# Optimization experiments

Measured on AMD Instinct MI355X. Metric: run time of the kernel, lower is better.

The kernel has to match this reference:

```python
import math
import jax, jax.numpy as jnp
import numpy as np

N, E, D, H, NH, DH, EIN, EOUT, G = 30000, 480000, 128, 128, 4, 32, 16, 16, 64
EPS = 1e-5

def _leaky(x):
    return jax.nn.leaky_relu(x, 0.01)

def _graph_norm(x, batch, w, b, a):
    # torch_geometric GraphNorm: out = w * (x - a*mean) / sqrt(var + eps) + b, stats per graph
    cnt = jnp.maximum(jax.ops.segment_sum(jnp.ones((x.shape[0],), x.dtype), batch, num_segments=G), 1.0)[:, None]
    mean = jax.ops.segment_sum(x, batch, num_segments=G) / cnt
    out = x - a * mean[batch]
    var = jax.ops.segment_sum(out * out, batch, num_segments=G) / cnt
    return w * out / jnp.sqrt(var + EPS)[batch] + b

def setup_inputs() -> dict:
    key = jax.random.key(0)
    ks = jax.random.split(key, 24)
    lin = lambda k, di, do: jax.random.normal(k, (di, do), jnp.float32) * 0.02
    z = lambda d: jnp.zeros((d,), jnp.float32)
    o = lambda d: jnp.ones((d,), jnp.float32)
    return {
        "node": jax.random.normal(ks[0], (N, D), jnp.float32),
        "edge": jax.random.normal(ks[1], (E, EIN), jnp.float32),
        "coords": jax.random.normal(ks[2], (N, 3), jnp.float32),
        "Ws": lin(ks[3], D, H), "bs": z(H),
        "Wd": lin(ks[4], D, H), "bd": z(H),
        "Wv": lin(ks[5], D, H), "bv": z(H),
        "We1": lin(ks[6], EIN + 1, H), "be1": z(H),
        "We2": lin(ks[7], H, H), "be2": z(H),
        "Wun": lin(ks[8], H, H), "bun": z(H),
        "Wue": lin(ks[9], H, EOUT), "bue": z(EOUT),
        "Wg": lin(ks[10], 3 * H, H), "bg": z(H),
        "Wf1": lin(ks[11], H, H), "bf1": z(H),
        "Wf2": lin(ks[12], H, H), "bf2": z(H),
        "gn1_w": o(H), "gn1_b": z(H), "gn1_a": o(H),
        "gn2_w": o(H), "gn2_b": z(H), "gn2_a": o(H),
        "edge_index": jax.random.randint(ks[13], (2, E), 0, N),
        "batch": jnp.sort(jax.random.randint(ks[14], (N,), 0, G)),
    }

def reference(node, edge, coords, Ws, bs, Wd, bd, Wv, bv, We1, be1, We2, be2,
              Wun, bun, Wue, bue, Wg, bg, Wf1, bf1, Wf2, bf2,
              gn1_w, gn1_b, gn1_a, gn2_w, gn2_b, gn2_a, edge_index, batch):
    i, j = edge_index[0], edge_index[1]
    src = node @ Ws + bs              # [N,H]
    dst = node @ Wd + bd
    value = node @ Wv + bv
    d = coords[i] - coords[j]
    dist = jnp.sqrt(jnp.sum(d * d, axis=-1, keepdims=True) + 1e-12) * 0.1
    e = jnp.concatenate([edge, dist], axis=-1)            # [E, EIN+1]
    e = _leaky(e @ We1 + be1) @ We2 + be2                   # edge_layer (dropout=identity in eval)
    edge_key = src[j] * e
    edge_result = (dst[i] * edge_key / math.sqrt(DH)).reshape(E, NH, DH)
    scores = jnp.sum(jnp.abs(edge_result), axis=2)         # L1 norm over dh -> [E,NH]
    smax = jax.ops.segment_max(scores, i, num_segments=N)  # scatter softmax over dst nodes
    ex = jnp.exp(scores - smax[i])
    den = jax.ops.segment_sum(ex, i, num_segments=N)
    ew = (ex / den[i])[..., None]                           # [E,NH,1]
    agg = jax.ops.segment_sum(ew * value[j].reshape(E, NH, DH), i, num_segments=N).reshape(N, H)
    node_new = agg @ Wun + bun
    edge_new = edge_result.reshape(E, H) @ Wue + bue
    g = jax.nn.sigmoid(jnp.concatenate([node_new, node, node_new - node], axis=-1) @ Wg + bg)
    n1 = _graph_norm(g * node_new + node, batch, gn1_w, gn1_b, gn1_a)
    fx = _leaky(n1 @ Wf1 + bf1) @ Wf2 + bf2                 # fix_node
    n2 = _graph_norm(g * fx + n1, batch, gn2_w, gn2_b, gn2_a)
    return (n2, edge_new, coords)
```

## Files before the change

kernel.cpp:

```cpp
#include <hip/hip_runtime.h>
#include <hip/hip_bf16.h>

#define NN_ 30000
#define NE_ 480000
#define DIM 128
#define EINF 16
#define EOUTF 16
#define NG 64
#define RSQRT_DH 0.17677669529663687f

typedef unsigned short u16;
typedef __attribute__((ext_vector_type(8))) short short8;
typedef __attribute__((ext_vector_type(8))) unsigned short ushort8v;
typedef __attribute__((ext_vector_type(4))) float floatx4;

#define W_DEG     0
#define W_CUR     30000
#define W_GSUM1   60000
#define W_GSQ1    68192
#define W_GSUM2   76384
#define W_GSQ2    84576
#define W_ZEND    92768
#define W_OFF     92768
#define W_BSUM    122772
#define W_GSTART  122900
#define W_EID     122968
#define W_JC      602968
#define W_SCORES  1082968
#define W_SRCB    3002968
#define W_DSTB    4922968
#define W_VALB    6842968
#define W_A       8762968
#define W_B       12602968
#define W_C       16442968
#define W_WGC     20282968
#define W_WE2B    20315736

static __device__ __forceinline__ u16 f2bf(float x) {
  __hip_bfloat16 h = __float2bfloat16(x);
  return *reinterpret_cast<u16*>(&h);
}
static __device__ __forceinline__ float bf2f(u16 v) {
  unsigned int b = ((unsigned int)v) << 16;
  return __uint_as_float(b);
}

static __device__ __forceinline__ void stage32(const float* __restrict__ X,
                                               float* xsb, int row0, int tid) {
#pragma unroll
  for (int t = 0; t < 4; ++t) {
    int idx = tid + t * 256;
    int r = idx >> 5, c4 = (idx & 31) * 4;
    int row = row0 + r;
    float4 v; v.x = v.y = v.z = v.w = 0.f;
    if (row < NN_) v = *(const float4*)&X[(size_t)row * DIM + c4];
    *(float4*)&xsb[r * DIM + c4] = v;
  }
}

static __device__ __forceinline__ void mm_k128(const float* xsb, int ld,
                                               const float* __restrict__ W,
                                               float acc[4][4], int tid) {
  int cg = tid & 31, rg = tid >> 5;
  int c0 = cg * 4, r0 = rg * 4;
  for (int k = 0; k < 128; k += 4) {
    float4 w0 = *(const float4*)&W[(size_t)(k + 0) * DIM + c0];
    float4 w1 = *(const float4*)&W[(size_t)(k + 1) * DIM + c0];
    float4 w2 = *(const float4*)&W[(size_t)(k + 2) * DIM + c0];
    float4 w3 = *(const float4*)&W[(size_t)(k + 3) * DIM + c0];
#pragma unroll
    for (int u = 0; u < 4; ++u) {
      float4 xv = *(const float4*)&xsb[(r0 + u) * ld + k];
      acc[u][0] += xv.x * w0.x + xv.y * w1.x + xv.z * w2.x + xv.w * w3.x;
      acc[u][1] += xv.x * w0.y + xv.y * w1.y + xv.z * w2.y + xv.w * w3.y;
      acc[u][2] += xv.x * w0.z + xv.y * w1.z + xv.z * w2.z + xv.w * w3.z;
      acc[u][3] += xv.x * w0.w + xv.y * w1.w + xv.z * w2.w + xv.w * w3.w;
    }
  }
}

static __device__ __forceinline__ void epi_store_bf(float acc[4][4],
    const float* __restrict__ bias, u16* __restrict__ Y,
    int row0, int tid) {
  int cg = tid & 31, rg = tid >> 5;
  int c0 = cg * 4, r0 = rg * 4;
  float4 bv = *(const float4*)&bias[c0];
#pragma unroll
  for (int u = 0; u < 4; ++u) {
    int row = row0 + r0 + u;
    if (row >= NN_) continue;
    ushort4 pk;
    pk.x = f2bf(acc[u][0] + bv.x); pk.y = f2bf(acc[u][1] + bv.y);
    pk.z = f2bf(acc[u][2] + bv.z); pk.w = f2bf(acc[u][3] + bv.w);
    *(ushort4*)&Y[(size_t)row * DIM + c0] = pk;
  }
}

static __device__ __forceinline__ void tile_gn_stats(const float* xsb,
    const int* bg_s, int row0, int tid,
    float* __restrict__ gsum, float* __restrict__ gsq) {
  int c = tid & 127, half = tid >> 7;
  float sm = 0.f, sq = 0.f;
  int gcur = -1;
  for (int r = 0; r < 16; ++r) {
    int rl = half * 16 + r;
    int row = row0 + rl;
    if (row >= NN_) break;
    int g = bg_s[rl];
    float v = xsb[rl * DIM + c];
    if (g != gcur) {
      if (gcur >= 0) {
        atomicAdd(&gsum[gcur * DIM + c], sm);
        atomicAdd(&gsq[gcur * DIM + c], sq);
      }
      gcur = g; sm = 0.f; sq = 0.f;
    }
    sm += v; sq += v * v;
  }
  if (gcur >= 0) {
    atomicAdd(&gsum[gcur * DIM + c], sm);
    atomicAdd(&gsq[gcur * DIM + c], sq);
  }
}

__global__ void setup_kernel(int* __restrict__ wsi, const int* __restrict__ batch,
                             int* __restrict__ gstart,
                             const float* __restrict__ Wg, float* __restrict__ Wgc,
                             const float* __restrict__ We2, u16* __restrict__ we2b) {
  int b = blockIdx.x, tid = threadIdx.x;
  if (b < 363) {
    int i = b * 256 + tid;
    if (i < W_ZEND) wsi[i] = 0;
  } else if (b == 363) {
    int g = tid;
    if (g <= NG) {
      int lo = 0, hi = NN_;
      while (lo < hi) { int mid = (lo + hi) >> 1; if (batch[mid] < g) lo = mid + 1; else hi = mid; }
      gstart[g] = lo;
    }
  } else if (b < 492) {
    int idx = (b - 364) * 256 + tid;
    int k = idx >> 7, c = idx & 127;
    float v;
    if (k < 128) v = Wg[(size_t)k * DIM + c] + Wg[(size_t)(256 + k) * DIM + c];
    else { int kk = k - 128; v = Wg[(size_t)(128 + kk) * DIM + c] - Wg[(size_t)(256 + kk) * DIM + c]; }
    Wgc[idx] = v;
  } else {
    int idx = (b - 492) * 256 + tid;
    if (idx < 16384) {
      int j = idx & 7, lane = (idx >> 3) & 63, s = (idx >> 9) & 3, T = idx >> 11;
      int k = s * 32 + ((lane >> 4) << 3) + j;
      int n = T * 16 + (lane & 15);
      we2b[idx] = f2bf(We2[(size_t)k * DIM + n]);
    }
  }
}

__global__ void deg_kernel(const int* __restrict__ EI, int* __restrict__ deg) {
  int e = blockIdx.x * 256 + threadIdx.x;
  if (e < NE_) atomicAdd(&deg[EI[e]], 1);
}

__global__ void __launch_bounds__(256) proj_kernel(
    const float* __restrict__ node,
    const float* __restrict__ Ws, const float* __restrict__ bs,
    const float* __restrict__ Wd, const float* __restrict__ bd,
    const float* __restrict__ Wv, const float* __restrict__ bv,
    u16* __restrict__ srcb, u16* __restrict__ dstb, u16* __restrict__ valb) {
  __shared__ __align__(16) float xs[32 * DIM];
  int tid = threadIdx.x, row0 = blockIdx.x * 32;
  stage32(node, xs, row0, tid);
  __syncthreads();
  const float* Wt[3] = {Ws, Wd, Wv};
  const float* Bt[3] = {bs, bd, bv};
  u16* Yt[3] = {srcb, dstb, valb};
#pragma unroll
  for (int w3 = 0; w3 < 3; ++w3) {
    float acc[4][4] = {};
    mm_k128(xs, DIM, Wt[w3], acc, tid);
    epi_store_bf(acc, Bt[w3], Yt[w3], row0, tid);
  }
}

__global__ void __launch_bounds__(256) nnew_gate_kernel(
    const float* __restrict__ AGG, const float* __restrict__ NODE,
    const int* __restrict__ batch,
    const float* __restrict__ Wun, const float* __restrict__ bun,
    const float* __restrict__ Wgc, const float* __restrict__ bg,
    float* __restrict__ gsum1, float* __restrict__ gsq1,
    float* __restrict__ G, float* __restrict__ X1) {
  __shared__ __align__(16) float xs0[32 * DIM];
  __shared__ __align__(16) float xs1[32 * DIM];
  __shared__ int bg_s[32];
  int tid = threadIdx.x, row0 = blockIdx.x * 32;
  stage32(AGG, xs0, row0, tid);
  stage32(NODE, xs1, row0, tid);
  if (tid < 32) {
    int row = row0 + tid;
    bg_s[tid] = (row < NN_) ? batch[row] : 0;
  }
  __syncthreads();
  int cg = tid & 31, rg = tid >> 5, c0 = cg * 4, r0 = rg * 4;
  {
    float acc[4][4] = {};
    mm_k128(xs0, DIM, Wun, acc, tid);
    __syncthreads();
    float4 bv = *(const float4*)&bun[c0];
#pragma unroll
    for (int u = 0; u < 4; ++u) {
      float4 ov; ov.x = acc[u][0] + bv.x; ov.y = acc[u][1] + bv.y;
      ov.z = acc[u][2] + bv.z; ov.w = acc[u][3] + bv.w;
      *(float4*)&xs0[(r0 + u) * DIM + c0] = ov;
    }
  }
  __syncthreads();
  float acc[4][4] = {};
  mm_k128(xs0, DIM, Wgc, acc, tid);
  mm_k128(xs1, DIM, Wgc + 128 * DIM, acc, tid);
  float4 bv = *(const float4*)&bg[c0];
  float4 xvv[4];
#pragma unroll
  for (int u = 0; u < 4; ++u) {
    int row = row0 + r0 + u;
    float z0 = acc[u][0] + bv.x, z1 = acc[u][1] + bv.y;
    float z2 = acc[u][2] + bv.z, z3 = acc[u][3] + bv.w;
    float g0 = 1.f / (1.f + __expf(-z0));
    float g1 = 1.f / (1.f + __expf(-z1));
    float g2 = 1.f / (1.f + __expf(-z2));
    float g3 = 1.f / (1.f + __expf(-z3));
    float4 nn4 = *(const float4*)&xs0[(r0 + u) * DIM + c0];
    float4 nd4 = *(const float4*)&xs1[(r0 + u) * DIM + c0];
    float4 gv; gv.x = g0; gv.y = g1; gv.z = g2; gv.w = g3;
    float4 xv; xv.x = g0 * nn4.x + nd4.x; xv.y = g1 * nn4.y + nd4.y;
    xv.z = g2 * nn4.z + nd4.z; xv.w = g3 * nn4.w + nd4.w;
    xvv[u] = xv;
    if (row < NN_) {
      *(float4*)&G[(size_t)row * DIM + c0] = gv;
      *(float4*)&X1[(size_t)row * DIM + c0] = xv;
    }
  }
  __syncthreads();
#pragma unroll
  for (int u = 0; u < 4; ++u)
    *(float4*)&xs1[(r0 + u) * DIM + c0] = xvv[u];
  __syncthreads();
  tile_gn_stats(xs1, bg_s, row0, tid, gsum1, gsq1);
}

__global__ void __launch_bounds__(256) fx_kernel(
    const float* __restrict__ X1, const int* __restrict__ batch,
    const int* __restrict__ gstart,
    const float* __restrict__ gsum1, const float* __restrict__ gsq1,
    const float* __restrict__ g1w, const float* __restrict__ g1b,
    const float* __restrict__ g1a,
    const float* __restrict__ Wf1, const float* __restrict__ bf1,
    const float* __restrict__ Wf2, const float* __restrict__ bf2,
    const float* __restrict__ G,
    float* __restrict__ gsum2, float* __restrict__ gsq2,
    float* __restrict__ X2) {
  __shared__ __align__(16) float xs0[32 * DIM];
  __shared__ __align__(16) float xs1[32 * DIM];
  __shared__ int bg_s[32];
  int tid = threadIdx.x, row0 = blockIdx.x * 32;
  stage32(X1, xs0, row0, tid);
  if (tid < 32) {
    int row = row0 + tid;
    bg_s[tid] = (row < NN_) ? batch[row] : 0;
  }
  __syncthreads();
  int cg = tid & 31, rg = tid >> 5, c0 = cg * 4, r0 = rg * 4;
#pragma unroll
  for (int u = 0; u < 4; ++u) {
    int rl = r0 + u, row = row0 + rl;
    if (row >= NN_) continue;
    int g = bg_s[rl];
    float cnt = fmaxf((float)(gstart[g + 1] - gstart[g]), 1.f);
    float inv = 1.f / cnt;
    float4 xv = *(const float4*)&xs0[rl * DIM + c0];
    float4 sm = *(const float4*)&gsum1[g * DIM + c0];
    float4 sq = *(const float4*)&gsq1[g * DIM + c0];
    float4 av = *(const float4*)&g1a[c0];
    float4 wv = *(const float4*)&g1w[c0];
    float4 bvv = *(const float4*)&g1b[c0];
    float4 ov;
    {
      float mean = sm.x * inv, msq = sq.x * inv, am = av.x * mean;
      float var = msq - 2.f * am * mean + am * am;
      ov.x = wv.x * (xv.x - am) * rsqrtf(var + 1e-5f) + bvv.x;
    }
    {
      float mean = sm.y * inv, msq = sq.y * inv, am = av.y * mean;
      float var = msq - 2.f * am * mean + am * am;
      ov.y = wv.y * (xv.y - am) * rsqrtf(var + 1e-5f) + bvv.y;
    }
    {
      float mean = sm.z * inv, msq = sq.z * inv, am = av.z * mean;
      float var = msq - 2.f * am * mean + am * am;
      ov.z = wv.z * (xv.z - am) * rsqrtf(var + 1e-5f) + bvv.z;
    }
    {
      float mean = sm.w * inv, msq = sq.w * inv, am = av.w * mean;
      float var = msq - 2.f * am * mean + am * am;
      ov.w = wv.w * (xv.w - am) * rsqrtf(var + 1e-5f) + bvv.w;
    }
    *(float4*)&xs0[rl * DIM + c0] = ov;
  }
  __syncthreads();
  {
    float acc[4][4] = {};
    mm_k128(xs0, DIM, Wf1, acc, tid);
    float4 bv = *(const float4*)&bf1[c0];
#pragma unroll
    for (int u = 0; u < 4; ++u) {
      float t0 = acc[u][0] + bv.x, t1 = acc[u][1] + bv.y;
      float t2 = acc[u][2] + bv.z, t3 = acc[u][3] + bv.w;
      t0 = t0 > 0.f ? t0 : 0.01f * t0; t1 = t1 > 0.f ? t1 : 0.01f * t1;
      t2 = t2 > 0.f ? t2 : 0.01f * t2; t3 = t3 > 0.f ? t3 : 0.01f * t3;
      float4 ov; ov.x = t0; ov.y = t1; ov.z = t2; ov.w = t3;
      *(float4*)&xs1[(r0 + u) * DIM + c0] = ov;
    }
  }
  __syncthreads();
  float acc[4][4] = {};
  mm_k128(xs1, DIM, Wf2, acc, tid);
  float4 bv = *(const float4*)&bf2[c0];
  float4 x2v[4];
#pragma unroll
  for (int u = 0; u < 4; ++u) {
    int row = row0 + r0 + u;
    float4 nv = *(const float4*)&xs0[(r0 + u) * DIM + c0];
    float4 gv; gv.x = gv.y = gv.z = gv.w = 0.f;
    if (row < NN_) gv = *(const float4*)&G[(size_t)row * DIM + c0];
    float4 ov;
    ov.x = gv.x * (acc[u][0] + bv.x) + nv.x;
    ov.y = gv.y * (acc[u][1] + bv.y) + nv.y;
    ov.z = gv.z * (acc[u][2] + bv.z) + nv.z;
    ov.w = gv.w * (acc[u][3] + bv.w) + nv.w;
    x2v[u] = ov;
    if (row < NN_) *(float4*)&X2[(size_t)row * DIM + c0] = ov;
  }
  __syncthreads();
#pragma unroll
  for (int u = 0; u < 4; ++u)
    *(float4*)&xs1[(r0 + u) * DIM + c0] = x2v[u];
  __syncthreads();
  tile_gn_stats(xs1, bg_s, row0, tid, gsum2, gsq2);
}

__global__ void scanA_kernel(const int* __restrict__ deg, int* __restrict__ off,
                             int* __restrict__ bsum) {
  __shared__ int buf[256];
  int tid = threadIdx.x;
  int i = blockIdx.x * 256 + tid;
  int v = (i < NN_) ? deg[i] : 0;
  buf[tid] = v;
  __syncthreads();
  for (int s = 1; s < 256; s <<= 1) {
    int t = (tid >= s) ? buf[tid - s] : 0;
    __syncthreads();
    buf[tid] += t;
    __syncthreads();
  }
  if (i < NN_) off[i] = buf[tid] - v;
  if (tid == 255) bsum[blockIdx.x] = buf[255];
}

__global__ void scanB_kernel(int* __restrict__ bsum) {
  const int NBLK = (NN_ + 255) / 256;
  __shared__ int buf[128];
  int tid = threadIdx.x;
  int v = (tid < NBLK) ? bsum[tid] : 0;
  buf[tid] = v;
  __syncthreads();
  for (int s = 1; s < 128; s <<= 1) {
    int t = (tid >= s) ? buf[tid - s] : 0;
    __syncthreads();
    buf[tid] += t;
    __syncthreads();
  }
  if (tid < NBLK) bsum[tid] = buf[tid] - v;
}

__global__ void scanC_kernel(int* __restrict__ off, const int* __restrict__ bsum) {
  int i = blockIdx.x * 256 + threadIdx.x;
  if (i < NN_) off[i] += bsum[i >> 8];
  if (i == 0) off[NN_] = NE_;
}

__global__ void fill_kernel(const int* __restrict__ EI, const int* __restrict__ off,
                            int* __restrict__ cur, int* __restrict__ eidb,
                            int* __restrict__ jcsr) {
  int e = blockIdx.x * 256 + threadIdx.x;
  if (e >= NE_) return;
  int i = EI[e];
  int p = atomicAdd(&cur[i], 1);
  int pos = off[i] + p;
  eidb[pos] = e;
  jcsr[pos] = EI[NE_ + e];
}

__global__ void __launch_bounds__(256, 5) edge_kernel(
    const float* __restrict__ edgef, const float* __restrict__ coords,
    const int* __restrict__ EI, const int* __restrict__ eidb,
    const float* __restrict__ We1, const float* __restrict__ be1,
    const float* __restrict__ be2, const u16* __restrict__ we2b,
    const float* __restrict__ Wue, const float* __restrict__ bue,
    const u16* __restrict__ srcb, const u16* __restrict__ dstb,
    float* __restrict__ scores, float* __restrict__ outE) {
  __shared__ __align__(16) float regA[2816];
  __shared__ __align__(16) float ers[32 * 132];
  __shared__ float bue_s[EOUTF];
  __shared__ int ii[32], jj[32], ee[32];

  float* xs   = regA;
  u16*   hbf  = (u16*)(regA + 640);
  float* wue_s= regA;

  int tid = threadIdx.x;
  int bid = blockIdx.x;
  int bswz = (bid & 7) * (NE_ / 32 / 8) + (bid >> 3);
  int p0 = bswz * 32;

  if (tid < 32) {
    int p = p0 + tid;
    int e = eidb[p];
    ee[tid] = e;
    int i = EI[e], j = EI[NE_ + e];
    ii[tid] = i; jj[tid] = j;
    float dx = coords[i * 3 + 0] - coords[j * 3 + 0];
    float dy = coords[i * 3 + 1] - coords[j * 3 + 1];
    float dz = coords[i * 3 + 2] - coords[j * 3 + 2];
    float dist = sqrtf(dx * dx + dy * dy + dz * dz + 1e-12f) * 0.1f;
    xs[tid * 20 + 16] = dist;
  }
  if (tid < EOUTF) bue_s[tid] = bue[tid];
  __syncthreads();

  if (tid < 128) {
    int r = tid >> 2, c4 = (tid & 3) * 4;
    *(float4*)&xs[r * 20 + c4] = *(const float4*)&edgef[(size_t)ee[r] * EINF + c4];
  }
  __syncthreads();

  int cg = tid & 31, rg = tid >> 5, c0 = cg * 4, r0 = rg * 4;

  {
    float acc[4][4] = {};
    for (int k = 0; k < 16; k += 4) {
      float4 w0 = *(const float4*)&We1[(size_t)(k + 0) * DIM + c0];
      float4 w1 = *(const float4*)&We1[(size_t)(k + 1) * DIM + c0];
      float4 w2 = *(const float4*)&We1[(size_t)(k + 2) * DIM + c0];
      float4 w3 = *(const float4*)&We1[(size_t)(k + 3) * DIM + c0];
#pragma unroll
      for (int u = 0; u < 4; ++u) {
        float4 xv = *(const float4*)&xs[(r0 + u) * 20 + k];
        acc[u][0] += xv.x * w0.x + xv.y * w1.x + xv.z * w2.x + xv.w * w3.x;
        acc[u][1] += xv.x * w0.y + xv.y * w1.y + xv.z * w2.y + xv.w * w3.y;
        acc[u][2] += xv.x * w0.z + xv.y * w1.z + xv.z * w2.z + xv.w * w3.z;
        acc[u][3] += xv.x * w0.w + xv.y * w1.w + xv.z * w2.w + xv.w * w3.w;
      }
    }
    {
      float4 w4 = *(const float4*)&We1[(size_t)16 * DIM + c0];
#pragma unroll
      for (int u = 0; u < 4; ++u) {
        float xd = xs[(r0 + u) * 20 + 16];
        acc[u][0] += xd * w4.x; acc[u][1] += xd * w4.y;
        acc[u][2] += xd * w4.z; acc[u][3] += xd * w4.w;
      }
    }
    float4 b1 = *(const float4*)&be1[c0];
#pragma unroll
    for (int u = 0; u < 4; ++u) {
      float h0 = acc[u][0] + b1.x, h1 = acc[u][1] + b1.y;
      float h2 = acc[u][2] + b1.z, h3 = acc[u][3] + b1.w;
      h0 = h0 > 0.f ? h0 : 0.01f * h0; h1 = h1 > 0.f ? h1 : 0.01f * h1;
      h2 = h2 > 0.f ? h2 : 0.01f * h2; h3 = h3 > 0.f ? h3 : 0.01f * h3;
      ushort4 pk; pk.x = f2bf(h0); pk.y = f2bf(h1); pk.z = f2bf(h2); pk.w = f2bf(h3);
      *(ushort4*)&hbf[(r0 + u) * 136 + c0] = pk;
    }
  }
  __syncthreads();

  int wv = tid >> 6, lane = tid & 63;
  int mtile = wv & 1, nhalf = wv >> 1;
  int quad = lane >> 4, lrow = lane & 15;
  int m0 = mtile * 16;

  short8 afrag[4];
#pragma unroll
  for (int s = 0; s < 4; ++s)
    afrag[s] = *(const short8*)&hbf[(m0 + lrow) * 136 + s * 32 + quad * 8];
  __syncthreads();

  for (int idx = tid; idx < 16 * DIM; idx += 256) {
    int oc = idx >> 7, k = idx & 127;
    wue_s[oc * 132 + k] = Wue[(size_t)k * EOUTF + oc];
  }

  floatx4 dacc[4];
#pragma unroll
  for (int t = 0; t < 4; ++t) dacc[t] = (floatx4){0.f, 0.f, 0.f, 0.f};
#pragma unroll
  for (int s = 0; s < 4; ++s) {
#pragma unroll
    for (int t = 0; t < 4; ++t) {
      int T = nhalf * 4 + t;
      short8 bfrg = *(const short8*)&we2b[(size_t)((T * 4 + s) * 64 + lane) * 8];
      dacc[t] = __builtin_amdgcn_mfma_f32_16x16x32_bf16(afrag[s], bfrg, dacc[t], 0, 0, 0);
    }
  }

#pragma unroll
  for (int t = 0; t < 4; ++t) {
    int col = nhalf * 64 + t * 16 + lrow;
    float b2v = be2[col];
#pragma unroll
    for (int r = 0; r < 4; ++r) {
      int erow = m0 + quad * 4 + r;
      ers[erow * 132 + col] = dacc[t][r] + b2v;
    }
  }
  __syncthreads();

  {
    int el2 = tid >> 3, cb2 = tid & 7;
    int c0b = cb2 * 16;
    int irow = ii[el2], jrow = jj[el2];
    ushort8v dv8a = *(const ushort8v*)&dstb[(size_t)irow * DIM + c0b];
    ushort8v dv8b = *(const ushort8v*)&dstb[(size_t)irow * DIM + c0b + 8];
    ushort8v sv8a = *(const ushort8v*)&srcb[(size_t)jrow * DIM + c0b];
    ushort8v sv8b = *(const ushort8v*)&srcb[(size_t)jrow * DIM + c0b + 8];

    float ef[16];
#pragma unroll
    for (int q = 0; q < 4; ++q) {
      float4 v = *(const float4*)&ers[el2 * 132 + c0b + q * 4];
      ef[q * 4 + 0] = v.x; ef[q * 4 + 1] = v.y;
      ef[q * 4 + 2] = v.z; ef[q * 4 + 3] = v.w;
    }
    float asum = 0.f;
#pragma unroll
    for (int k = 0; k < 8; ++k) {
      float er = bf2f((u16)dv8a[k]) * bf2f((u16)sv8a[k]) * ef[k] * RSQRT_DH;
      ef[k] = er; asum += fabsf(er);
    }
#pragma unroll
    for (int k = 0; k < 8; ++k) {
      float er = bf2f((u16)dv8b[k]) * bf2f((u16)sv8b[k]) * ef[8 + k] * RSQRT_DH;
      ef[8 + k] = er; asum += fabsf(er);
    }
#pragma unroll
    for (int q = 0; q < 4; ++q) {
      float4 v; v.x = ef[q * 4 + 0]; v.y = ef[q * 4 + 1];
      v.z = ef[q * 4 + 2]; v.w = ef[q * 4 + 3];
      *(float4*)&ers[el2 * 132 + c0b + q * 4] = v;
    }
    asum += __shfl_xor(asum, 1);
    if ((cb2 & 1) == 0)
      scores[(size_t)(p0 + el2) * 4 + (cb2 >> 1)] = asum;
  }
  __syncthreads();

  int el = tid >> 3, oc2 = (tid & 7) * 2;
  float a0 = 0.f, a1 = 0.f;
  for (int k = 0; k < DIM; k += 4) {
    float4 e4 = *(const float4*)&ers[el * 132 + k];
    float4 w0 = *(const float4*)&wue_s[oc2 * 132 + k];
    float4 w1 = *(const float4*)&wue_s[(oc2 + 1) * 132 + k];
    a0 += e4.x * w0.x + e4.y * w0.y + e4.z * w0.z + e4.w * w0.w;
    a1 += e4.x * w1.x + e4.y * w1.y + e4.z * w1.z + e4.w * w1.w;
  }
  size_t ob = (size_t)ee[el] * EOUTF + oc2;
  float2 o2; o2.x = a0 + bue_s[oc2]; o2.y = a1 + bue_s[oc2 + 1];
  *(float2*)&outE[ob] = o2;
}

__global__ void __launch_bounds__(256) agg_kernel(
    const u16* __restrict__ valb, const float* __restrict__ scores,
    const int* __restrict__ off, const int* __restrict__ jcsr,
    float* __restrict__ agg) {
  int n = blockIdx.x * 4 + (threadIdx.x >> 6);
  int l = threadIdx.x & 63;
  if (n >= NN_) return;
  int s = off[n], e_end = off[n + 1];

  float m0 = -1e30f, m1 = -1e30f, m2 = -1e30f, m3 = -1e30f;
  for (int p = s + l; p < e_end; p += 64) {
    float4 sc = *(const float4*)&scores[(size_t)p * 4];
    m0 = fmaxf(m0, sc.x); m1 = fmaxf(m1, sc.y);
    m2 = fmaxf(m2, sc.z); m3 = fmaxf(m3, sc.w);
  }
#pragma unroll
  for (int d = 1; d < 64; d <<= 1) {
    m0 = fmaxf(m0, __shfl_xor(m0, d)); m1 = fmaxf(m1, __shfl_xor(m1, d));
    m2 = fmaxf(m2, __shfl_xor(m2, d)); m3 = fmaxf(m3, __shfl_xor(m3, d));
  }
  int hh = l >> 4;
  float mh = (hh == 0) ? m0 : (hh == 1) ? m1 : (hh == 2) ? m2 : m3;

  float acc0 = 0.f, acc1 = 0.f, den = 0.f;
  int p = s;
  for (; p + 2 <= e_end; p += 2) {
    int j0 = jcsr[p], j1 = jcsr[p + 1];
    float s0 = scores[(size_t)p * 4 + hh];
    float s1 = scores[(size_t)(p + 1) * 4 + hh];
    ushort2 u0 = *(const ushort2*)&valb[(size_t)j0 * DIM + 2 * l];
    ushort2 u1 = *(const ushort2*)&valb[(size_t)j1 * DIM + 2 * l];
    float e0 = __expf(s0 - mh), e1 = __expf(s1 - mh);
    den += e0 + e1;
    acc0 += e0 * bf2f(u0.x) + e1 * bf2f(u1.x);
    acc1 += e0 * bf2f(u0.y) + e1 * bf2f(u1.y);
  }
  if (p < e_end) {
    int j = jcsr[p];
    float s0 = scores[(size_t)p * 4 + hh];
    ushort2 u0 = *(const ushort2*)&valb[(size_t)j * DIM + 2 * l];
    float e0 = __expf(s0 - mh);
    den += e0;
    acc0 += e0 * bf2f(u0.x);
    acc1 += e0 * bf2f(u0.y);
  }
  float2 o;
  if (e_end > s) { o.x = acc0 / den; o.y = acc1 / den; }
  else { o.x = 0.f; o.y = 0.f; }
  *(float2*)&agg[(size_t)n * DIM + 2 * l] = o;
}

__global__ void gn_apply_kernel(const float* __restrict__ X, const int* __restrict__ batch,
    const int* __restrict__ gstart, const float* __restrict__ gsum,
    const float* __restrict__ gsq, const float* __restrict__ w,
    const float* __restrict__ b, const float* __restrict__ a,
    float* __restrict__ Y) {
  int idx = blockIdx.x * 256 + threadIdx.x;
  if (idx >= NN_ * 32) return;
  int n = idx >> 5, c4 = (idx & 31) * 4;
  int g = batch[n];
  float cnt = fmaxf((float)(gstart[g + 1] - gstart[g]), 1.f);
  float inv = 1.f / cnt;
  float4 xv = *(const float4*)&X[(size_t)n * DIM + c4];
  float4 sm = *(const float4*)&gsum[g * DIM + c4];
  float4 sq = *(const float4*)&gsq[g * DIM + c4];
  float4 av = *(const float4*)&a[c4];
  float4 wv = *(const float4*)&w[c4];
  float4 bv = *(const float4*)&b[c4];
  float4 ov;
  {
    float mean = sm.x * inv, msq = sq.x * inv, am = av.x * mean;
    float var = msq - 2.f * am * mean + am * am;
    ov.x = wv.x * (xv.x - am) * rsqrtf(var + 1e-5f) + bv.x;
  }
  {
    float mean = sm.y * inv, msq = sq.y * inv, am = av.y * mean;
    float var = msq - 2.f * am * mean + am * am;
    ov.y = wv.y * (xv.y - am) * rsqrtf(var + 1e-5f) + bv.y;
  }
  {
    float mean = sm.z * inv, msq = sq.z * inv, am = av.z * mean;
    float var = msq - 2.f * am * mean + am * am;
    ov.z = wv.z * (xv.z - am) * rsqrtf(var + 1e-5f) + bv.z;
  }
  {
    float mean = sm.w * inv, msq = sq.w * inv, am = av.w * mean;
    float var = msq - 2.f * am * mean + am * am;
    ov.w = wv.w * (xv.w - am) * rsqrtf(var + 1e-5f) + bv.w;
  }
  *(float4*)&Y[(size_t)n * DIM + c4] = ov;
}

__global__ void coords_kernel(const float* __restrict__ C, float* __restrict__ O) {
  int i = blockIdx.x * 256 + threadIdx.x;
  if (i < NN_ * 3) O[i] = C[i];
}

extern "C" void kernel_launch(void* const* d_in, const int* in_sizes, int n_in,
                              void* d_out, int out_size, void* d_ws, size_t ws_size,
                              hipStream_t stream) {
  (void)in_sizes; (void)n_in; (void)out_size; (void)ws_size;
  const float* node  = (const float*)d_in[0];
  const float* edgef = (const float*)d_in[1];
  const float* coords= (const float*)d_in[2];
  const float* Ws  = (const float*)d_in[3];  const float* bs  = (const float*)d_in[4];
  const float* Wd  = (const float*)d_in[5];  const float* bd  = (const float*)d_in[6];
  const float* Wv  = (const float*)d_in[7];  const float* bv  = (const float*)d_in[8];
  const float* We1 = (const float*)d_in[9];  const float* be1 = (const float*)d_in[10];
  const float* We2 = (const float*)d_in[11]; const float* be2 = (const float*)d_in[12];
  const float* Wun = (const float*)d_in[13]; const float* bun = (const float*)d_in[14];
  const float* Wue = (const float*)d_in[15]; const float* bue = (const float*)d_in[16];
  const float* Wg  = (const float*)d_in[17]; const float* bg  = (const float*)d_in[18];
  const float* Wf1 = (const float*)d_in[19]; const float* bf1 = (const float*)d_in[20];
  const float* Wf2 = (const float*)d_in[21]; const float* bf2 = (const float*)d_in[22];
  const float* g1w = (const float*)d_in[23]; const float* g1b = (const float*)d_in[24];
  const float* g1a = (const float*)d_in[25];
  const float* g2w = (const float*)d_in[26]; const float* g2b = (const float*)d_in[27];
  const float* g2a = (const float*)d_in[28];
  const int* EI    = (const int*)d_in[29];
  const int* batch = (const int*)d_in[30];
  float* out = (float*)d_out;

  int*   wsi = (int*)d_ws;
  float* wsf = (float*)d_ws;
  int* deg    = wsi + W_DEG;
  int* cur    = wsi + W_CUR;
  int* offs   = wsi + W_OFF;
  int* bsum   = wsi + W_BSUM;
  int* gstart = wsi + W_GSTART;
  int* eidb   = wsi + W_EID;
  int* jcsr   = wsi + W_JC;
  float* gsum1 = wsf + W_GSUM1; float* gsq1 = wsf + W_GSQ1;
  float* gsum2 = wsf + W_GSUM2; float* gsq2 = wsf + W_GSQ2;
  float* scores_ = wsf + W_SCORES;
  u16* srcb = (u16*)(wsf + W_SRCB);
  u16* dstb = (u16*)(wsf + W_DSTB);
  u16* valb = (u16*)(wsf + W_VALB);
  float* A = wsf + W_A;
  float* B = wsf + W_B;
  float* wgc_ = wsf + W_WGC;
  u16*   we2b = (u16*)(wsf + W_WE2B);

  float* outE = out + (size_t)NN_ * DIM;
  float* outC = out + (size_t)NN_ * DIM + (size_t)NE_ * EOUTF;

  setup_kernel<<<556, 256, 0, stream>>>(wsi, batch, gstart, Wg, wgc_, We2, we2b);
  deg_kernel<<<(NE_ + 255) / 256, 256, 0, stream>>>(EI, deg);
  scanA_kernel<<<(NN_ + 255) / 256, 256, 0, stream>>>(deg, offs, bsum);
  scanB_kernel<<<1, 128, 0, stream>>>(bsum);
  scanC_kernel<<<(NN_ + 255) / 256, 256, 0, stream>>>(offs, bsum);
  fill_kernel<<<(NE_ + 255) / 256, 256, 0, stream>>>(EI, offs, cur, eidb, jcsr);
  proj_kernel<<<(NN_ + 31) / 32, 256, 0, stream>>>(node, Ws, bs, Wd, bd, Wv, bv,
                                                   srcb, dstb, valb);
  edge_kernel<<<NE_ / 32, 256, 0, stream>>>(edgef, coords, EI, eidb, We1, be1,
                                            be2, we2b, Wue, bue,
                                            srcb, dstb, scores_, outE);
  agg_kernel<<<NN_ / 4, 256, 0, stream>>>(valb, scores_, offs, jcsr, A);
  nnew_gate_kernel<<<(NN_ + 31) / 32, 256, 0, stream>>>(A, node, batch, Wun, bun,
                                                        wgc_, bg, gsum1, gsq1, B, A);
  fx_kernel<<<(NN_ + 31) / 32, 256, 0, stream>>>(A, batch, gstart, gsum1, gsq1,
                                                 g1w, g1b, g1a, Wf1, bf1, Wf2, bf2,
                                                 B, gsum2, gsq2, A);
  gn_apply_kernel<<<(NN_ * 32 + 255) / 256, 256, 0, stream>>>(
      A, batch, gstart, gsum2, gsq2, g2w, g2b, g2a, out);
  coords_kernel<<<(NN_ * 3 + 255) / 256, 256, 0, stream>>>(coords, outC);
}
```

Measured before the change: 605.8 us.

## Use split-bf16 MFMA for node projections, unroll aggregation, merge small kernels

The node projection GEMM moves from scalar fp32 FMAs to bf16 MFMA. Both activations and weights are split into hi/lo bf16 parts and combined with three MFMAs to keep near-fp32 accuracy, and the weights are pre-swizzled in setup. The aggregation loop is unrolled from 2 to 4 edges to expose more memory-level parallelism. Workspace zeroing moves to hipMemsetAsync, and the coords copy is folded into the gn_apply kernel, which removes one launch; the MFMA path adds an LDS staging round-trip and extra syncs.

New measurement: 574.0 us. 1.06x faster.

```diff
diff --git a/kernel.cpp b/kernel.cpp
--- a/kernel.cpp
+++ b/kernel.cpp
@@ -35,6 +35,7 @@
 #define W_C       16442968
 #define W_WGC     20282968
 #define W_WE2B    20315736
+#define W_WPROJ   20323928
 
 static __device__ __forceinline__ u16 f2bf(float x) {
   __hip_bfloat16 h = __float2bfloat16(x);
@@ -76,23 +77,6 @@
       acc[u][2] += xv.x * w0.z + xv.y * w1.z + xv.z * w2.z + xv.w * w3.z;
       acc[u][3] += xv.x * w0.w + xv.y * w1.w + xv.z * w2.w + xv.w * w3.w;
     }
-  }
-}
-
-static __device__ __forceinline__ void epi_store_bf(float acc[4][4],
-    const float* __restrict__ bias, u16* __restrict__ Y,
-    int row0, int tid) {
-  int cg = tid & 31, rg = tid >> 5;
-  int c0 = cg * 4, r0 = rg * 4;
-  float4 bv = *(const float4*)&bias[c0];
-#pragma unroll
-  for (int u = 0; u < 4; ++u) {
-    int row = row0 + r0 + u;
-    if (row >= NN_) continue;
-    ushort4 pk;
-    pk.x = f2bf(acc[u][0] + bv.x); pk.y = f2bf(acc[u][1] + bv.y);
-    pk.z = f2bf(acc[u][2] + bv.z); pk.w = f2bf(acc[u][3] + bv.w);
-    *(ushort4*)&Y[(size_t)row * DIM + c0] = pk;
   }
 }
 
@@ -123,36 +107,45 @@
   }
 }
 
-__global__ void setup_kernel(int* __restrict__ wsi, const int* __restrict__ batch,
-                             int* __restrict__ gstart,
+__global__ void setup_kernel(const int* __restrict__ batch, int* __restrict__ gstart,
                              const float* __restrict__ Wg, float* __restrict__ Wgc,
-                             const float* __restrict__ We2, u16* __restrict__ we2b) {
+                             const float* __restrict__ We2, u16* __restrict__ we2b,
+                             const float* __restrict__ Ws, const float* __restrict__ Wd,
+                             const float* __restrict__ Wv, u16* __restrict__ wproj) {
   int b = blockIdx.x, tid = threadIdx.x;
-  if (b < 363) {
-    int i = b * 256 + tid;
-    if (i < W_ZEND) wsi[i] = 0;
-  } else if (b == 363) {
+  if (b == 0) {
     int g = tid;
     if (g <= NG) {
       int lo = 0, hi = NN_;
       while (lo < hi) { int mid = (lo + hi) >> 1; if (batch[mid] < g) lo = mid + 1; else hi = mid; }
       gstart[g] = lo;
     }
-  } else if (b < 492) {
-    int idx = (b - 364) * 256 + tid;
+  } else if (b < 129) {
+    int idx = (b - 1) * 256 + tid;
     int k = idx >> 7, c = idx & 127;
     float v;
     if (k < 128) v = Wg[(size_t)k * DIM + c] + Wg[(size_t)(256 + k) * DIM + c];
     else { int kk = k - 128; v = Wg[(size_t)(128 + kk) * DIM + c] - Wg[(size_t)(256 + kk) * DIM + c]; }
     Wgc[idx] = v;
+  } else if (b < 193) {
+    int idx = (b - 129) * 256 + tid;
+    int j = idx & 7, lane = (idx >> 3) & 63, s = (idx >> 9) & 3, T = idx >> 11;
+    int k = s * 32 + ((lane >> 4) << 3) + j;
+    int n = T * 16 + (lane & 15);
+    we2b[idx] = f2bf(We2[(size_t)k * DIM + n]);
   } else {
-    int idx = (b - 492) * 256 + tid;
-    if (idx < 16384) {
-      int j = idx & 7, lane = (idx >> 3) & 63, s = (idx >> 9) & 3, T = idx >> 11;
-      int k = s * 32 + ((lane >> 4) << 3) + j;
-      int n = T * 16 + (lane & 15);
-      we2b[idx] = f2bf(We2[(size_t)k * DIM + n]);
-    }
+    int idx = (b - 193) * 256 + tid;
+    int which = idx >> 14;
+    int sub = idx & 16383;
+    int j = sub & 7, lane = (sub >> 3) & 63, s = (sub >> 9) & 3, T = sub >> 11;
+    int k = s * 32 + ((lane >> 4) << 3) + j;
+    int n = T * 16 + (lane & 15);
+    int mat = which >> 1;
+    const float* Wsrc = (mat == 0) ? Ws : (mat == 1) ? Wd : Wv;
+    float w = Wsrc[(size_t)k * DIM + n];
+    u16 h = f2bf(w);
+    u16 o = (which & 1) ? f2bf(w - bf2f(h)) : h;
+    wproj[which * 16384 + sub] = o;
   }
 }
 
@@ -162,23 +155,104 @@
 }
 
 __global__ void __launch_bounds__(256) proj_kernel(
-    const float* __restrict__ node,
-    const float* __restrict__ Ws, const float* __restrict__ bs,
-    const float* __restrict__ Wd, const float* __restrict__ bd,
-    const float* __restrict__ Wv, const float* __restrict__ bv,
+    const float* __restrict__ node, const u16* __restrict__ wproj,
+    const float* __restrict__ bs, const float* __restrict__ bd,
+    const float* __restrict__ bv,
     u16* __restrict__ srcb, u16* __restrict__ dstb, u16* __restrict__ valb) {
-  __shared__ __align__(16) float xs[32 * DIM];
+  __shared__ __align__(16) u16 ah[32 * 136];
+  __shared__ __align__(16) u16 al[32 * 136];
+  __shared__ __align__(16) float park[32 * 132];
   int tid = threadIdx.x, row0 = blockIdx.x * 32;
-  stage32(node, xs, row0, tid);
-  __syncthreads();
-  const float* Wt[3] = {Ws, Wd, Wv};
+  int r2 = tid >> 3, c16 = (tid & 7) * 16;
+
+  {
+    int row = row0 + r2;
+    float v[16];
+    if (row < NN_) {
+#pragma unroll
+      for (int q = 0; q < 4; ++q) {
+        float4 x = *(const float4*)&node[(size_t)row * DIM + c16 + q * 4];
+        v[q * 4 + 0] = x.x; v[q * 4 + 1] = x.y;
+        v[q * 4 + 2] = x.z; v[q * 4 + 3] = x.w;
+      }
+    } else {
+#pragma unroll
+      for (int q = 0; q < 16; ++q) v[q] = 0.f;
+    }
+#pragma unroll
+    for (int h2 = 0; h2 < 2; ++h2) {
+      ushort8v hh, ll;
+#pragma unroll
+      for (int q = 0; q < 8; ++q) {
+        float x = v[h2 * 8 + q];
+        u16 h = f2bf(x);
+        hh[q] = h;
+        ll[q] = f2bf(x - bf2f(h));
+      }
+      *(ushort8v*)&ah[r2 * 136 + c16 + h2 * 8] = hh;
+      *(ushort8v*)&al[r2 * 136 + c16 + h2 * 8] = ll;
+    }
+  }
+  __syncthreads();
+
+  int wv_ = tid >> 6, lane = tid & 63;
+  int mtile = wv_ & 1, nhalf = wv_ >> 1;
+  int quad = lane >> 4, lrow = lane & 15;
+  int m0 = mtile * 16;
+
+  short8 afh[4], afl[4];
+#pragma unroll
+  for (int s = 0; s < 4; ++s) {
+    afh[s] = *(const short8*)&ah[(m0 + lrow) * 136 + s * 32 + quad * 8];
+    afl[s] = *(const short8*)&al[(m0 + lrow) * 136 + s * 32 + quad * 8];
+  }
+
   const float* Bt[3] = {bs, bd, bv};
   u16* Yt[3] = {srcb, dstb, valb};
-#pragma unroll
-  for (int w3 = 0; w3 < 3; ++w3) {
-    float acc[4][4] = {};
-    mm_k128(xs, DIM, Wt[w3], acc, tid);
-    epi_store_bf(acc, Bt[w3], Yt[w3], row0, tid);
+#pragma unroll 1
+  for (int g3 = 0; g3 < 3; ++g3) {
+    const u16* wh = wproj + (size_t)(g3 * 2 + 0) * 16384;
+    const u16* wl = wproj + (size_t)(g3 * 2 + 1) * 16384;
+    floatx4 dacc[4];
+#pragma unroll
+    for (int t = 0; t < 4; ++t) dacc[t] = (floatx4){0.f, 0.f, 0.f, 0.f};
+#pragma unroll
+    for (int s = 0; s < 4; ++s) {
+#pragma unroll
+      for (int t = 0; t < 4; ++t) {
+        int T = nhalf * 4 + t;
+        size_t off = (size_t)((T * 4 + s) * 64 + lane) * 8;
+        short8 bh = *(const short8*)&wh[off];
+        short8 bl = *(const short8*)&wl[off];
+        dacc[t] = __builtin_amdgcn_mfma_f32_16x16x32_bf16(afh[s], bh, dacc[t], 0, 0, 0);
+        dacc[t] = __builtin_amdgcn_mfma_f32_16x16x32_bf16(afl[s], bh, dacc[t], 0, 0, 0);
+        dacc[t] = __builtin_amdgcn_mfma_f32_16x16x32_bf16(afh[s], bl, dacc[t], 0, 0, 0);
+      }
+    }
+#pragma unroll
+    for (int t = 0; t < 4; ++t) {
+      int col = nhalf * 64 + t * 16 + lrow;
+#pragma unroll
+      for (int r = 0; r < 4; ++r)
+        park[(m0 + quad * 4 + r) * 132 + col] = dacc[t][r];
+    }
+    __syncthreads();
+    {
+      int row = row0 + r2;
+      if (row < NN_) {
+#pragma unroll
+        for (int h2 = 0; h2 < 2; ++h2) {
+          ushort8v o;
+#pragma unroll
+          for (int q = 0; q < 8; ++q) {
+            float pv = park[r2 * 132 + c16 + h2 * 8 + q] + Bt[g3][c16 + h2 * 8 + q];
+            o[q] = f2bf(pv);
+          }
+          *(ushort8v*)&Yt[g3][(size_t)row * DIM + c16 + h2 * 8] = o;
+        }
+      }
+    }
+    __syncthreads();
   }
 }
 
@@ -601,18 +675,23 @@
 
   float acc0 = 0.f, acc1 = 0.f, den = 0.f;
   int p = s;
-  for (; p + 2 <= e_end; p += 2) {
-    int j0 = jcsr[p], j1 = jcsr[p + 1];
+  for (; p + 4 <= e_end; p += 4) {
+    int j0 = jcsr[p], j1 = jcsr[p + 1], j2 = jcsr[p + 2], j3 = jcsr[p + 3];
     float s0 = scores[(size_t)p * 4 + hh];
     float s1 = scores[(size_t)(p + 1) * 4 + hh];
+    float s2 = scores[(size_t)(p + 2) * 4 + hh];
+    float s3 = scores[(size_t)(p + 3) * 4 + hh];
     ushort2 u0 = *(const ushort2*)&valb[(size_t)j0 * DIM + 2 * l];
     ushort2 u1 = *(const ushort2*)&valb[(size_t)j1 * DIM + 2 * l];
+    ushort2 u2 = *(const ushort2*)&valb[(size_t)j2 * DIM + 2 * l];
+    ushort2 u3 = *(const ushort2*)&valb[(size_t)j3 * DIM + 2 * l];
     float e0 = __expf(s0 - mh), e1 = __expf(s1 - mh);
-    den += e0 + e1;
-    acc0 += e0 * bf2f(u0.x) + e1 * bf2f(u1.x);
-    acc1 += e0 * bf2f(u0.y) + e1 * bf2f(u1.y);
-  }
-  if (p < e_end) {
+    float e2 = __expf(s2 - mh), e3 = __expf(s3 - mh);
+    den += (e0 + e1) + (e2 + e3);
+    acc0 += e0 * bf2f(u0.x) + e1 * bf2f(u1.x) + e2 * bf2f(u2.x) + e3 * bf2f(u3.x);
+    acc1 += e0 * bf2f(u0.y) + e1 * bf2f(u1.y) + e2 * bf2f(u2.y) + e3 * bf2f(u3.y);
+  }
+  for (; p < e_end; ++p) {
     int j = jcsr[p];
     float s0 = scores[(size_t)p * 4 + hh];
     ushort2 u0 = *(const ushort2*)&valb[(size_t)j * DIM + 2 * l];
@@ -631,9 +710,15 @@
     const int* __restrict__ gstart, const float* __restrict__ gsum,
     const float* __restrict__ gsq, const float* __restrict__ w,
     const float* __restrict__ b, const float* __restrict__ a,
-    float* __restrict__ Y) {
-  int idx = blockIdx.x * 256 + threadIdx.x;
-  if (idx >= NN_ * 32) return;
+    float* __restrict__ Y,
+    const float* __restrict__ C, float* __restrict__ OC) {
+  int blk = blockIdx.x;
+  if (blk >= (NN_ * 32) / 256) {
+    int i = (blk - (NN_ * 32) / 256) * 256 + threadIdx.x;
+    if (i < NN_ * 3) OC[i] = C[i];
+    return;
+  }
+  int idx = blk * 256 + threadIdx.x;
   int n = idx >> 5, c4 = (idx & 31) * 4;
   int g = batch[n];
   float cnt = fmaxf((float)(gstart[g + 1] - gstart[g]), 1.f);
@@ -666,11 +751,6 @@
     ov.w = wv.w * (xv.w - am) * rsqrtf(var + 1e-5f) + bv.w;
   }
   *(float4*)&Y[(size_t)n * DIM + c4] = ov;
-}
-
-__global__ void coords_kernel(const float* __restrict__ C, float* __restrict__ O) {
-  int i = blockIdx.x * 256 + threadIdx.x;
-  if (i < NN_ * 3) O[i] = C[i];
 }
 
 extern "C" void kernel_launch(void* const* d_in, const int* in_sizes, int n_in,
@@ -717,17 +797,20 @@
   float* B = wsf + W_B;
   float* wgc_ = wsf + W_WGC;
   u16*   we2b = (u16*)(wsf + W_WE2B);
+  u16*   wproj = (u16*)(wsf + W_WPROJ);
 
   float* outE = out + (size_t)NN_ * DIM;
   float* outC = out + (size_t)NN_ * DIM + (size_t)NE_ * EOUTF;
 
-  setup_kernel<<<556, 256, 0, stream>>>(wsi, batch, gstart, Wg, wgc_, We2, we2b);
+  hipMemsetAsync(d_ws, 0, (size_t)W_ZEND * sizeof(int), stream);
+  setup_kernel<<<577, 256, 0, stream>>>(batch, gstart, Wg, wgc_, We2, we2b,
+                                        Ws, Wd, Wv, wproj);
   deg_kernel<<<(NE_ + 255) / 256, 256, 0, stream>>>(EI, deg);
   scanA_kernel<<<(NN_ + 255) / 256, 256, 0, stream>>>(deg, offs, bsum);
   scanB_kernel<<<1, 128, 0, stream>>>(bsum);
   scanC_kernel<<<(NN_ + 255) / 256, 256, 0, stream>>>(offs, bsum);
   fill_kernel<<<(NE_ + 255) / 256, 256, 0, stream>>>(EI, offs, cur, eidb, jcsr);
-  proj_kernel<<<(NN_ + 31) / 32, 256, 0, stream>>>(node, Ws, bs, Wd, bd, Wv, bv,
+  proj_kernel<<<(NN_ + 31) / 32, 256, 0, stream>>>(node, wproj, bs, bd, bv,
                                                    srcb, dstb, valb);
   edge_kernel<<<NE_ / 32, 256, 0, stream>>>(edgef, coords, EI, eidb, We1, be1,
                                             be2, we2b, Wue, bue,
@@ -738,7 +821,6 @@
   fx_kernel<<<(NN_ + 31) / 32, 256, 0, stream>>>(A, batch, gstart, gsum1, gsq1,
                                                  g1w, g1b, g1a, Wf1, bf1, Wf2, bf2,
                                                  B, gsum2, gsq2, A);
-  gn_apply_kernel<<<(NN_ * 32 + 255) / 256, 256, 0, stream>>>(
-      A, batch, gstart, gsum2, gsq2, g2w, g2b, g2a, out);
-  coords_kernel<<<(NN_ * 3 + 255) / 256, 256, 0, stream>>>(coords, outC);
-}
+  gn_apply_kernel<<<(NN_ * 32) / 256 + (NN_ * 3 + 255) / 256, 256, 0, stream>>>(
+      A, batch, gstart, gsum2, gsq2, g2w, g2b, g2a, out, coords, outC);
+}
```
